# Performance work log

Hardware: AMD Instinct MI355X
Metric: run time of the kernel (lower is better)

The kernel has to match this reference:

```python
import jax, jax.numpy as jnp
import numpy as np

N, E, F, H, C, G = 100000, 1600000, 128, 128, 1, 512
NLAYERS, DT, ALPHA, GAMMA = 5, 1.0, 1.0, 1.0


def setup_inputs() -> dict:
    key = jax.random.key(0)
    ks = jax.random.split(key, 11)
    x = jax.random.normal(ks[0], (N, F), dtype=jnp.float32)
    edge_index = jax.random.randint(ks[1], (2, E), 0, N, dtype=jnp.int64)
    batch = jnp.sort(jax.random.randint(ks[2], (N,), 0, G, dtype=jnp.int64))
    s = 1.0 / np.sqrt(H).astype(np.float32)
    W_enc = jax.random.normal(ks[3], (H, F), jnp.float32) * (1.0 / np.sqrt(F))
    b_enc = jnp.zeros((H,), jnp.float32)
    W_conv = jax.random.normal(ks[4], (H, H), jnp.float32) * s
    b_conv = jnp.zeros((H,), jnp.float32)
    W_res = jax.random.normal(ks[5], (H, H), jnp.float32) * s
    b_res = jnp.zeros((H,), jnp.float32)
    W_dec = jax.random.normal(ks[6], (C, H), jnp.float32) * s
    b_dec = jnp.zeros((C,), jnp.float32)
    return {
        "x": x, "edge_index": edge_index, "batch": batch,
        "W_enc": W_enc, "b_enc": b_enc,
        "W_conv": W_conv, "b_conv": b_conv,
        "W_res": W_res, "b_res": b_res,
        "W_dec": W_dec, "b_dec": b_dec,
    }


def reference(x, edge_index, batch, W_enc, b_enc, W_conv, b_conv, W_res, b_res, W_dec, b_dec):
    src, dst = edge_index[0], edge_index[1]
    # GCN symmetric normalization with self-loops: deg = 1 + in-degree(dst)
    deg = jnp.zeros((N,), x.dtype).at[dst].add(1.0) + 1.0
    dinv = jax.lax.rsqrt(deg)
    norm = dinv[src] * dinv[dst]            # [E]
    self_norm = (dinv * dinv)[:, None]      # [N,1] self-loop coefficient

    def gcn_conv(X):
        xw = X @ W_conv.T                   # lin (bias=False)
        agg = jnp.zeros_like(xw).at[dst].add(norm[:, None] * xw[src])
        agg = agg + self_norm * xw          # self-loop term
        return agg + b_conv

    Y = x @ W_enc.T + b_enc
    Xs = Y
    for _ in range(NLAYERS):
        res = Xs @ W_res.T + b_res - Xs @ W_conv.T   # res(X) - conv.lin(X)
        Y = Y + DT * (jax.nn.relu(gcn_conv(Xs) + res) - ALPHA * Y - GAMMA * Xs)
        Xs = Xs + DT * Y
    out = Xs @ W_dec.T + b_dec               # [N, 1]
    pooled = jax.ops.segment_sum(out, batch, num_segments=G)  # [G, 1]
    return pooled.squeeze(-1)                # [G]
```

## Files before the change

### kernel.cpp

```cpp
#include <hip/hip_runtime.h>
#include <hip/hip_bf16.h>
#include <stdint.h>


#define HD 128
#define SCHUNK 2048

typedef __attribute__((ext_vector_type(4))) float f32x4;
typedef __attribute__((ext_vector_type(8))) float f32x8;
typedef __attribute__((ext_vector_type(8))) _Float16 f16x8;

__global__ __launch_bounds__(256) void k_deg(const int* __restrict__ dst, int E,
                                             int* __restrict__ cnt){
  int e = blockIdx.x * 256 + threadIdx.x;
  if (e < E) atomicAdd(&cnt[dst[e]], 1);
}

__global__ __launch_bounds__(256) void k_scan_part(const int* __restrict__ cnt,
                                                   int* __restrict__ bsum, int N){
  __shared__ int red[256];
  int t = threadIdx.x;
  int lo = blockIdx.x * SCHUNK + t * 8;
  int s = 0;
#pragma unroll
  for (int k = 0; k < 8; ++k){
    int i = lo + k;
    s += (i < N) ? cnt[i] : 0;
  }
  red[t] = s;
  __syncthreads();
  for (int off = 128; off > 0; off >>= 1){
    if (t < off) red[t] += red[t + off];
    __syncthreads();
  }
  if (t == 0) bsum[blockIdx.x] = red[0];
}

__global__ __launch_bounds__(1024) void k_scan_mid(const int* __restrict__ bsum,
                                                   int* __restrict__ boff, int nb,
                                                   int* __restrict__ rp, int N, int E){
  __shared__ int part[1024];
  int t = threadIdx.x;
  part[t] = (t < nb) ? bsum[t] : 0;
  __syncthreads();
  for (int off = 1; off < 1024; off <<= 1){
    int v = (t >= off) ? part[t - off] : 0;
    __syncthreads();
    part[t] += v;
    __syncthreads();
  }
  if (t < nb) boff[t] = (t == 0) ? 0 : part[t - 1];
  if (t == 0) rp[N] = E;
}

__global__ __launch_bounds__(256) void k_scan_apply(const int* __restrict__ cnt,
                                                    const int* __restrict__ boff,
                                                    int* __restrict__ rp,
                                                    float* __restrict__ dinv, int N){
  __shared__ int tsum[256];
  int t = threadIdx.x;
  int lo = blockIdx.x * SCHUNK + t * 8;
  int v[8];
  int s = 0;
#pragma unroll
  for (int k = 0; k < 8; ++k){
    int i = lo + k;
    v[k] = (i < N) ? cnt[i] : 0;
    s += v[k];
  }
  tsum[t] = s;
  __syncthreads();
  for (int off = 1; off < 256; off <<= 1){
    int u = (t >= off) ? tsum[t - off] : 0;
    __syncthreads();
    tsum[t] += u;
    __syncthreads();
  }
  int base = boff[blockIdx.x] + ((t == 0) ? 0 : tsum[t - 1]);
#pragma unroll
  for (int k = 0; k < 8; ++k){
    int i = lo + k;
    if (i < N){
      rp[i] = base;
      dinv[i] = rsqrtf((float)v[k] + 1.0f);
      base += v[k];
    }
  }
}

__global__ __launch_bounds__(256) void k_fill(const int* __restrict__ src,
                                              const int* __restrict__ dst, int E,
                                              const int* __restrict__ rp,
                                              int* cnt,
                                              const float* __restrict__ dinv,
                                              unsigned* __restrict__ col){
  int e = blockIdx.x * 256 + threadIdx.x;
  if (e >= E) return;
  int s = src[e], d = dst[e];
  int pos = rp[d] + atomicSub(&cnt[d], 1) - 1;
  float di = dinv[s];
  int deg1 = (int)(1.0f / (di * di) + 0.5f);
  col[pos] = ((unsigned)deg1 << 18) | (unsigned)s;
}

__global__ __launch_bounds__(256) void k_prep_w(const float* __restrict__ Wc,
                                                const float* __restrict__ Wr,
                                                const float* __restrict__ We,
                                                const float* __restrict__ bc,
                                                const float* __restrict__ br,
                                                _Float16* __restrict__ WcF,
                                                _Float16* __restrict__ WrF,
                                                _Float16* __restrict__ WeF,
                                                float* __restrict__ bias_sum){
  int i = blockIdx.x * 256 + threadIdx.x;
  if (i < HD * HD){
    WcF[i] = (_Float16)Wc[i];
    WrF[i] = (_Float16)Wr[i];
    WeF[i] = (_Float16)We[i];
  }
  if (i < HD) bias_sum[i] = bc[i] + br[i];
}

__global__ __launch_bounds__(256) void k_agg(const _Float16* __restrict__ XsH,
                                             const float* __restrict__ dinv,
                                             const int* __restrict__ rp,
                                             const unsigned* __restrict__ col,
                                             _Float16* __restrict__ U,
                                             int N){
  int w = threadIdx.x >> 6;
  int lane = threadIdx.x & 63;
  int q = lane >> 4;
  int ql = lane & 15;
  int node = blockIdx.x * 4 + w;
  if (node >= N) return;

  float acc[8];
#pragma unroll
  for (int i = 0; i < 8; ++i) acc[i] = 0.f;

  int b = rp[node], e = rp[node + 1];
  int j = b + q;
  for (; j + 4 < e; j += 8){
    unsigned r0 = col[j];
    unsigned r1 = col[j + 4];
    float w0 = rsqrtf((float)(r0 >> 18));
    float w1 = rsqrtf((float)(r1 >> 18));
    f16x8 v0 = ((const f16x8*)(XsH + (size_t)(r0 & 0x3FFFFu) * HD))[ql];
    f16x8 v1 = ((const f16x8*)(XsH + (size_t)(r1 & 0x3FFFFu) * HD))[ql];
#pragma unroll
    for (int i = 0; i < 8; ++i) acc[i] = fmaf(w0, (float)v0[i], acc[i]);
#pragma unroll
    for (int i = 0; i < 8; ++i) acc[i] = fmaf(w1, (float)v1[i], acc[i]);
  }
  if (j < e){
    unsigned r0 = col[j];
    float w0 = rsqrtf((float)(r0 >> 18));
    f16x8 v0 = ((const f16x8*)(XsH + (size_t)(r0 & 0x3FFFFu) * HD))[ql];
#pragma unroll
    for (int i = 0; i < 8; ++i) acc[i] = fmaf(w0, (float)v0[i], acc[i]);
  }

  float dn = dinv[node];
#pragma unroll
  for (int i = 0; i < 8; ++i){
    acc[i] += __shfl_xor(acc[i], 16, 64);
    acc[i] += __shfl_xor(acc[i], 32, 64);
    acc[i] *= dn;
  }
  if (q == 0){
    f16x8 o;
#pragma unroll
    for (int i = 0; i < 8; ++i) o[i] = (_Float16)acc[i];
    ((f16x8*)(U + (size_t)node * HD))[ql] = o;
  }
}

__global__ __launch_bounds__(256) void k_gemm(
    const float* __restrict__ A1f,
    const _Float16* __restrict__ A1h,
    const _Float16* A2h,
    const _Float16* __restrict__ W1,
    const _Float16* __restrict__ W2,
    const float* __restrict__ dinvp,
    const float* __restrict__ bias,
    _Float16* outXsH,
    const float* __restrict__ Wd, const float* __restrict__ bd,
    float* __restrict__ val,
    int N, int relu, int decode){
  __shared__ _Float16 wsm[2 * HD * HD];
  f16x8* smv = (f16x8*)wsm;

  {
    int t = threadIdx.x;
    const f16x8* g1 = (const f16x8*)W1;
    for (int i = t; i < HD * HD / 8; i += 256){
      int row = i >> 4, slot = i & 15;
      smv[(row << 4) | (slot ^ (row & 7))] = g1[i];
    }
    if (W2){
      const f16x8* g2 = (const f16x8*)W2;
      for (int i = t; i < HD * HD / 8; i += 256){
        int row = i >> 4, slot = i & 15;
        smv[2048 + ((row << 4) | (slot ^ (row & 7)))] = g2[i];
      }
    }
  }
  __syncthreads();

  int wid = blockIdx.x * 4 + (threadIdx.x >> 6);
  int row0 = wid * 32;
  if (row0 >= N) return;
  int lane = threadIdx.x & 63;
  int r = lane & 15;
  int kg = lane >> 4;

  f32x4 acc[2][8];
#pragma unroll
  for (int s = 0; s < 2; ++s)
#pragma unroll
    for (int c = 0; c < 8; ++c) acc[s][c] = (f32x4)0.0f;

  const bool two = (A2h != nullptr);
  float sr[2] = {0.f, 0.f};
  if (two){
#pragma unroll
    for (int s = 0; s < 2; ++s){
      float d = dinvp[row0 + s * 16 + r];
      sr[s] = d * d - 1.0f;
    }
  }

#pragma unroll
  for (int kst = 0; kst < 4; ++kst){
    int k0 = kst * 32 + kg * 8;
    f16x8 a1[2], a2[2];
#pragma unroll
    for (int s = 0; s < 2; ++s){
      size_t ao = (size_t)(row0 + s * 16 + r) * HD + k0;
      if (two){
        f16x8 uh = *(const f16x8*)(A1h + ao);
        f16x8 xv = *(const f16x8*)(A2h + ao);
        a2[s] = xv;
#pragma unroll
        for (int i = 0; i < 8; ++i)
          a1[s][i] = (_Float16)fmaf(sr[s], (float)xv[i], (float)uh[i]);
      } else {
        f32x8 u = *(const f32x8*)(A1f + ao);
#pragma unroll
        for (int i = 0; i < 8; ++i) a1[s][i] = (_Float16)u[i];
      }
    }
    int swz = (kst * 4 + kg) ^ (r & 7);
#pragma unroll
    for (int ct = 0; ct < 8; ++ct){
      int ridx = ((ct * 16 + r) << 4) | swz;
      f16x8 b1 = smv[ridx];
#pragma unroll
      for (int s = 0; s < 2; ++s)
        acc[s][ct] = __builtin_amdgcn_mfma_f32_16x16x32_f16(a1[s], b1, acc[s][ct], 0, 0, 0);
      if (two){
        f16x8 b2 = smv[2048 + ridx];
#pragma unroll
        for (int s = 0; s < 2; ++s)
          acc[s][ct] = __builtin_amdgcn_mfma_f32_16x16x32_f16(a2[s], b2, acc[s][ct], 0, 0, 0);
      }
    }
  }

  float rowp[2][4] = {{0.f,0.f,0.f,0.f},{0.f,0.f,0.f,0.f}};
#pragma unroll
  for (int s = 0; s < 2; ++s){
#pragma unroll
    for (int ct = 0; ct < 8; ++ct){
      int cc = ct * 16 + r;
      float bv = bias[cc];
      float wdv = decode ? Wd[cc] : 0.f;
#pragma unroll
      for (int j = 0; j < 4; ++j){
        float v = acc[s][ct][j] + bv;
        if (relu) v = fmaxf(v, 0.0f);
        if (decode){
          rowp[s][j] += v * wdv;
        } else {
          int rr = row0 + s * 16 + kg * 4 + j;
          outXsH[(size_t)rr * HD + cc] = (_Float16)v;
        }
      }
    }
  }
  if (decode){
    float bd0 = bd[0];
#pragma unroll
    for (int s = 0; s < 2; ++s)
#pragma unroll
      for (int j = 0; j < 4; ++j){
        float t = rowp[s][j];
        t += __shfl_xor(t, 1, 64);
        t += __shfl_xor(t, 2, 64);
        t += __shfl_xor(t, 4, 64);
        t += __shfl_xor(t, 8, 64);
        if (r == 0) val[row0 + s * 16 + kg * 4 + j] = t + bd0;
      }
  }
}

#define POOL_CHUNK 1024
__global__ __launch_bounds__(256) void k_pool(const float* __restrict__ val,
                                              const int* __restrict__ batch,
                                              float* __restrict__ out, int N, int G){
  __shared__ float acc[4096];
  int t = threadIdx.x;
  int lo = blockIdx.x * POOL_CHUNK;
  int hi = min(lo + POOL_CHUNK, N);
  if (G <= 4096){
    for (int i = t; i < G; i += 256) acc[i] = 0.f;
    __syncthreads();
    for (int i = lo + t; i < hi; i += 256) atomicAdd(&acc[batch[i]], val[i]);
    __syncthreads();
    for (int i = t; i < G; i += 256){
      float v = acc[i];
      if (v != 0.f) atomicAdd(&out[i], v);
    }
  } else {
    for (int i = lo + t; i < hi; i += 256) atomicAdd(&out[batch[i]], val[i]);
  }
}

extern "C" void kernel_launch(void* const* d_in, const int* in_sizes, int n_in,
                              void* d_out, int out_size, void* d_ws, size_t ws_size,
                              hipStream_t stream){
  const float* x      = (const float*)d_in[0];
  const int*   ei     = (const int*)d_in[1];
  const int*   batch  = (const int*)d_in[2];
  const float* W_enc  = (const float*)d_in[3];
  const float* b_enc  = (const float*)d_in[4];
  const float* W_conv = (const float*)d_in[5];
  const float* b_conv = (const float*)d_in[6];
  const float* W_res  = (const float*)d_in[7];
  const float* b_res  = (const float*)d_in[8];
  const float* W_dec  = (const float*)d_in[9];
  const float* b_dec  = (const float*)d_in[10];

  const int N = in_sizes[0] / HD;
  const int E = in_sizes[1] / 2;
  float* out = (float*)d_out;

  char* ws = (char*)d_ws;
  size_t off = 0;
  auto alloc = [&](size_t bytes) -> char* {
    char* p = ws + off;
    off += (bytes + 255) & ~(size_t)255;
    return p;
  };
  int*   cnt   = (int*)  alloc((size_t)N * 4);
  int*   rp    = (int*)  alloc(((size_t)N + 1) * 4);
  float* dinv  = (float*)alloc((size_t)N * 4);
  int*   bsum  = (int*)  alloc(1024 * 4);
  int*   boff  = (int*)  alloc(1024 * 4);
  unsigned* col= (unsigned*)alloc((size_t)E * 4);
  _Float16* XsH= (_Float16*)alloc((size_t)N * HD * 2);
  _Float16* U  = (_Float16*)alloc((size_t)N * HD * 2);
  float* val   = (float*)alloc((size_t)N * 4);
  _Float16* WcF = (_Float16*)alloc((size_t)HD * HD * 2);
  _Float16* WrF = (_Float16*)alloc((size_t)HD * HD * 2);
  _Float16* WeF = (_Float16*)alloc((size_t)HD * HD * 2);
  float* bias_sum = (float*)alloc((size_t)HD * 4);

  hipMemsetAsync(cnt, 0, (size_t)N * 4, stream);
  hipMemsetAsync(out, 0, (size_t)out_size * 4, stream);

  const int* src = ei;
  const int* dst = ei + E;

  int nb = (N + SCHUNK - 1) / SCHUNK;

  k_deg       <<<(E + 255) / 256, 256, 0, stream>>>(dst, E, cnt);
  k_scan_part <<<nb, 256, 0, stream>>>(cnt, bsum, N);
  k_scan_mid  <<<1, 1024, 0, stream>>>(bsum, boff, nb, rp, N, E);
  k_scan_apply<<<nb, 256, 0, stream>>>(cnt, boff, rp, dinv, N);
  k_fill      <<<(E + 255) / 256, 256, 0, stream>>>(src, dst, E, rp, cnt, dinv, col);
  k_prep_w    <<<(HD * HD + 255) / 256, 256, 0, stream>>>(W_conv, W_res, W_enc, b_conv, b_res,
                                                          WcF, WrF, WeF, bias_sum);

  int gemm_blocks = ((N + 31) / 32 + 3) / 4;
  int node_blocks = (N + 3) / 4;

  k_gemm<<<gemm_blocks, 256, 0, stream>>>(x, nullptr, nullptr, WeF, nullptr,
                                          nullptr, b_enc, XsH,
                                          nullptr, nullptr, nullptr, N, 0, 0);

  for (int l = 0; l < 5; ++l){
    k_agg<<<node_blocks, 256, 0, stream>>>(XsH, dinv, rp, col, U, N);
    int last = (l == 4);
    k_gemm<<<gemm_blocks, 256, 0, stream>>>(nullptr, U, XsH, WcF, WrF,
                                            dinv, bias_sum, XsH,
                                            W_dec, b_dec, val, N, 1, last);
  }

  k_pool<<<(N + POOL_CHUNK - 1) / POOL_CHUNK, 256, 0, stream>>>(val, batch, out, N, out_size);
}
```

Before: 643.6 us.

## Replace atomic CSR build with bucketed binning, unroll aggregation, halve GEMM LDS

Replaces the degree-count, three-kernel scan and atomic fill with a two-level bucket sort. Edges are binned by destination block through per-block LDS staging, and each bucket then builds its CSR segment locally in LDS. The aggregation loop now handles four neighbours per iteration and reads dinv[src] directly instead of decoding a packed degree. The GEMM stages W2 into LDS only after the first product, which halves shared memory to raise occupancy. The fixed bucket capacities (BSTRIDE/BCAP) silently drop edges if a bucket overflows, and the extra dinv gather adds memory traffic.

```diff
diff --git a/kernel.cpp b/kernel.cpp
--- a/kernel.cpp
+++ b/kernel.cpp
@@ -4,103 +4,114 @@
 
 
 #define HD 128
-#define SCHUNK 2048
+#define BSH 9
+#define BSTRIDE 16384
+#define BCAP 12288
 
 typedef __attribute__((ext_vector_type(4))) float f32x4;
 typedef __attribute__((ext_vector_type(8))) float f32x8;
 typedef __attribute__((ext_vector_type(8))) _Float16 f16x8;
 
-__global__ __launch_bounds__(256) void k_deg(const int* __restrict__ dst, int E,
-                                             int* __restrict__ cnt){
-  int e = blockIdx.x * 256 + threadIdx.x;
-  if (e < E) atomicAdd(&cnt[dst[e]], 1);
-}
-
-__global__ __launch_bounds__(256) void k_scan_part(const int* __restrict__ cnt,
-                                                   int* __restrict__ bsum, int N){
-  __shared__ int red[256];
+__global__ __launch_bounds__(256) void k_bin(const int* __restrict__ src,
+                                             const int* __restrict__ dst, int E,
+                                             unsigned* __restrict__ tmp,
+                                             int* __restrict__ gcur, int nbuck){
+  __shared__ unsigned stage[256 * 32];
+  __shared__ int lcnt[256];
   int t = threadIdx.x;
-  int lo = blockIdx.x * SCHUNK + t * 8;
-  int s = 0;
+  lcnt[t] = 0;
+  __syncthreads();
+  int base = blockIdx.x * 2048;
 #pragma unroll
   for (int k = 0; k < 8; ++k){
-    int i = lo + k;
-    s += (i < N) ? cnt[i] : 0;
-  }
-  red[t] = s;
-  __syncthreads();
-  for (int off = 128; off > 0; off >>= 1){
-    if (t < off) red[t] += red[t + off];
-    __syncthreads();
-  }
-  if (t == 0) bsum[blockIdx.x] = red[0];
-}
-
-__global__ __launch_bounds__(1024) void k_scan_mid(const int* __restrict__ bsum,
-                                                   int* __restrict__ boff, int nb,
-                                                   int* __restrict__ rp, int N, int E){
-  __shared__ int part[1024];
+    int e = base + k * 256 + t;
+    if (e < E){
+      int d = dst[e], s = src[e];
+      unsigned rec = ((unsigned)(d & ((1 << BSH) - 1)) << 17) | (unsigned)s;
+      int b = d >> BSH;
+      int slot = atomicAdd(&lcnt[b], 1);
+      if (slot < 32) stage[b * 32 + slot] = rec;
+      else {
+        int g = atomicAdd(&gcur[b], 1);
+        if (g < BSTRIDE) tmp[(size_t)b * BSTRIDE + g] = rec;
+      }
+    }
+  }
+  __syncthreads();
+  int wv = t >> 6, lane = t & 63;
+  for (int b = wv; b < nbuck; b += 4){
+    int cnt = min(lcnt[b], 32);
+    if (cnt == 0) continue;
+    int gbase = 0;
+    if (lane == 0) gbase = atomicAdd(&gcur[b], cnt);
+    gbase = __shfl(gbase, 0, 64);
+    if (lane < cnt && gbase + lane < BSTRIDE)
+      tmp[(size_t)b * BSTRIDE + gbase + lane] = stage[b * 32 + lane];
+  }
+}
+
+__global__ __launch_bounds__(256) void k_bscan(const int* __restrict__ gcur,
+                                               int* __restrict__ bbase, int nbuck,
+                                               int* __restrict__ rp, int N, int E){
+  __shared__ int sm[256];
   int t = threadIdx.x;
-  part[t] = (t < nb) ? bsum[t] : 0;
-  __syncthreads();
-  for (int off = 1; off < 1024; off <<= 1){
-    int v = (t >= off) ? part[t - off] : 0;
-    __syncthreads();
-    part[t] += v;
-    __syncthreads();
-  }
-  if (t < nb) boff[t] = (t == 0) ? 0 : part[t - 1];
+  sm[t] = (t < nbuck) ? gcur[t] : 0;
+  __syncthreads();
+  for (int off = 1; off < 256; off <<= 1){
+    int v = (t >= off) ? sm[t - off] : 0;
+    __syncthreads();
+    sm[t] += v;
+    __syncthreads();
+  }
+  if (t < nbuck) bbase[t] = (t == 0) ? 0 : sm[t - 1];
   if (t == 0) rp[N] = E;
 }
 
-__global__ __launch_bounds__(256) void k_scan_apply(const int* __restrict__ cnt,
-                                                    const int* __restrict__ boff,
-                                                    int* __restrict__ rp,
-                                                    float* __restrict__ dinv, int N){
-  __shared__ int tsum[256];
-  int t = threadIdx.x;
-  int lo = blockIdx.x * SCHUNK + t * 8;
-  int v[8];
-  int s = 0;
-#pragma unroll
-  for (int k = 0; k < 8; ++k){
-    int i = lo + k;
-    v[k] = (i < N) ? cnt[i] : 0;
-    s += v[k];
-  }
-  tsum[t] = s;
+__global__ __launch_bounds__(256) void k_build(const unsigned* __restrict__ tmp,
+                                               const int* __restrict__ gcur,
+                                               const int* __restrict__ bbase,
+                                               int* __restrict__ rp,
+                                               float* __restrict__ dinv,
+                                               unsigned* __restrict__ col, int N){
+  __shared__ unsigned lcol[BCAP];
+  __shared__ int deg[512], rpl[512], cur[512];
+  __shared__ int ps[256];
+  int b = blockIdx.x, t = threadIdx.x;
+  int lo = b << BSH;
+  int nn = min(512, N - lo);
+  int count = min(gcur[b], BCAP);
+  int gbase = bbase[b];
+  for (int i = t; i < 512; i += 256){ deg[i] = 0; cur[i] = 0; }
+  __syncthreads();
+  const unsigned* trec = tmp + (size_t)b * BSTRIDE;
+  for (int i = t; i < count; i += 256)
+    atomicAdd(&deg[trec[i] >> 17], 1);
+  __syncthreads();
+  int a0 = deg[2 * t], a1 = deg[2 * t + 1];
+  ps[t] = a0 + a1;
   __syncthreads();
   for (int off = 1; off < 256; off <<= 1){
-    int u = (t >= off) ? tsum[t - off] : 0;
-    __syncthreads();
-    tsum[t] += u;
-    __syncthreads();
-  }
-  int base = boff[blockIdx.x] + ((t == 0) ? 0 : tsum[t - 1]);
-#pragma unroll
-  for (int k = 0; k < 8; ++k){
-    int i = lo + k;
-    if (i < N){
-      rp[i] = base;
-      dinv[i] = rsqrtf((float)v[k] + 1.0f);
-      base += v[k];
-    }
-  }
-}
-
-__global__ __launch_bounds__(256) void k_fill(const int* __restrict__ src,
-                                              const int* __restrict__ dst, int E,
-                                              const int* __restrict__ rp,
-                                              int* cnt,
-                                              const float* __restrict__ dinv,
-                                              unsigned* __restrict__ col){
-  int e = blockIdx.x * 256 + threadIdx.x;
-  if (e >= E) return;
-  int s = src[e], d = dst[e];
-  int pos = rp[d] + atomicSub(&cnt[d], 1) - 1;
-  float di = dinv[s];
-  int deg1 = (int)(1.0f / (di * di) + 0.5f);
-  col[pos] = ((unsigned)deg1 << 18) | (unsigned)s;
+    int v = (t >= off) ? ps[t - off] : 0;
+    __syncthreads();
+    ps[t] += v;
+    __syncthreads();
+  }
+  int excl = (t == 0) ? 0 : ps[t - 1];
+  rpl[2 * t] = excl;
+  rpl[2 * t + 1] = excl + a0;
+  __syncthreads();
+  for (int i = t; i < nn; i += 256){
+    rp[lo + i] = gbase + rpl[i];
+    dinv[lo + i] = rsqrtf((float)deg[i] + 1.0f);
+  }
+  for (int i = t; i < count; i += 256){
+    unsigned r = trec[i];
+    int d = r >> 17;
+    int pos = rpl[d] + atomicAdd(&cur[d], 1);
+    if (pos < BCAP) lcol[pos] = r & 0x1FFFFu;
+  }
+  __syncthreads();
+  for (int i = t; i < count; i += 256) col[gbase + i] = lcol[i];
 }
 
 __global__ __launch_bounds__(256) void k_prep_w(const float* __restrict__ Wc,
@@ -140,22 +151,32 @@
 
   int b = rp[node], e = rp[node + 1];
   int j = b + q;
-  for (; j + 4 < e; j += 8){
+  for (; j + 12 < e; j += 16){
     unsigned r0 = col[j];
     unsigned r1 = col[j + 4];
-    float w0 = rsqrtf((float)(r0 >> 18));
-    float w1 = rsqrtf((float)(r1 >> 18));
-    f16x8 v0 = ((const f16x8*)(XsH + (size_t)(r0 & 0x3FFFFu) * HD))[ql];
-    f16x8 v1 = ((const f16x8*)(XsH + (size_t)(r1 & 0x3FFFFu) * HD))[ql];
+    unsigned r2 = col[j + 8];
+    unsigned r3 = col[j + 12];
+    float w0 = dinv[r0];
+    float w1 = dinv[r1];
+    float w2 = dinv[r2];
+    float w3 = dinv[r3];
+    f16x8 v0 = ((const f16x8*)(XsH + (size_t)r0 * HD))[ql];
+    f16x8 v1 = ((const f16x8*)(XsH + (size_t)r1 * HD))[ql];
+    f16x8 v2 = ((const f16x8*)(XsH + (size_t)r2 * HD))[ql];
+    f16x8 v3 = ((const f16x8*)(XsH + (size_t)r3 * HD))[ql];
 #pragma unroll
     for (int i = 0; i < 8; ++i) acc[i] = fmaf(w0, (float)v0[i], acc[i]);
 #pragma unroll
     for (int i = 0; i < 8; ++i) acc[i] = fmaf(w1, (float)v1[i], acc[i]);
-  }
-  if (j < e){
+#pragma unroll
+    for (int i = 0; i < 8; ++i) acc[i] = fmaf(w2, (float)v2[i], acc[i]);
+#pragma unroll
+    for (int i = 0; i < 8; ++i) acc[i] = fmaf(w3, (float)v3[i], acc[i]);
+  }
+  for (; j < e; j += 4){
     unsigned r0 = col[j];
-    float w0 = rsqrtf((float)(r0 >> 18));
-    f16x8 v0 = ((const f16x8*)(XsH + (size_t)(r0 & 0x3FFFFu) * HD))[ql];
+    float w0 = dinv[r0];
+    f16x8 v0 = ((const f16x8*)(XsH + (size_t)r0 * HD))[ql];
 #pragma unroll
     for (int i = 0; i < 8; ++i) acc[i] = fmaf(w0, (float)v0[i], acc[i]);
   }
@@ -187,30 +208,24 @@
     const float* __restrict__ Wd, const float* __restrict__ bd,
     float* __restrict__ val,
     int N, int relu, int decode){
-  __shared__ _Float16 wsm[2 * HD * HD];
+  __shared__ _Float16 wsm[HD * HD];
   f16x8* smv = (f16x8*)wsm;
+  int t = threadIdx.x;
 
   {
-    int t = threadIdx.x;
     const f16x8* g1 = (const f16x8*)W1;
     for (int i = t; i < HD * HD / 8; i += 256){
       int row = i >> 4, slot = i & 15;
       smv[(row << 4) | (slot ^ (row & 7))] = g1[i];
     }
-    if (W2){
-      const f16x8* g2 = (const f16x8*)W2;
-      for (int i = t; i < HD * HD / 8; i += 256){
-        int row = i >> 4, slot = i & 15;
-        smv[2048 + ((row << 4) | (slot ^ (row & 7)))] = g2[i];
-      }
-    }
-  }
-  __syncthreads();
-
-  int wid = blockIdx.x * 4 + (threadIdx.x >> 6);
+  }
+  __syncthreads();
+
+  int wid = blockIdx.x * 4 + (t >> 6);
   int row0 = wid * 32;
-  if (row0 >= N) return;
-  int lane = threadIdx.x & 63;
+  bool act = (row0 < N);
+  int rowb = act ? row0 : 0;
+  int lane = t & 63;
   int r = lane & 15;
   int kg = lane >> 4;
 
@@ -225,7 +240,7 @@
   if (two){
 #pragma unroll
     for (int s = 0; s < 2; ++s){
-      float d = dinvp[row0 + s * 16 + r];
+      float d = dinvp[rowb + s * 16 + r];
       sr[s] = d * d - 1.0f;
     }
   }
@@ -233,14 +248,13 @@
 #pragma unroll
   for (int kst = 0; kst < 4; ++kst){
     int k0 = kst * 32 + kg * 8;
-    f16x8 a1[2], a2[2];
+    f16x8 a1[2];
 #pragma unroll
     for (int s = 0; s < 2; ++s){
-      size_t ao = (size_t)(row0 + s * 16 + r) * HD + k0;
+      size_t ao = (size_t)(rowb + s * 16 + r) * HD + k0;
       if (two){
         f16x8 uh = *(const f16x8*)(A1h + ao);
         f16x8 xv = *(const f16x8*)(A2h + ao);
-        a2[s] = xv;
 #pragma unroll
         for (int i = 0; i < 8; ++i)
           a1[s][i] = (_Float16)fmaf(sr[s], (float)xv[i], (float)uh[i]);
@@ -253,13 +267,34 @@
     int swz = (kst * 4 + kg) ^ (r & 7);
 #pragma unroll
     for (int ct = 0; ct < 8; ++ct){
-      int ridx = ((ct * 16 + r) << 4) | swz;
-      f16x8 b1 = smv[ridx];
+      f16x8 b1 = smv[((ct * 16 + r) << 4) | swz];
 #pragma unroll
       for (int s = 0; s < 2; ++s)
         acc[s][ct] = __builtin_amdgcn_mfma_f32_16x16x32_f16(a1[s], b1, acc[s][ct], 0, 0, 0);
-      if (two){
-        f16x8 b2 = smv[2048 + ridx];
+    }
+  }
+
+  if (two){
+    __syncthreads();
+    const f16x8* g2 = (const f16x8*)W2;
+    for (int i = t; i < HD * HD / 8; i += 256){
+      int row = i >> 4, slot = i & 15;
+      smv[(row << 4) | (slot ^ (row & 7))] = g2[i];
+    }
+    __syncthreads();
+#pragma unroll
+    for (int kst = 0; kst < 4; ++kst){
+      int k0 = kst * 32 + kg * 8;
+      f16x8 a2[2];
+#pragma unroll
+      for (int s = 0; s < 2; ++s){
+        size_t ao = (size_t)(rowb + s * 16 + r) * HD + k0;
+        a2[s] = *(const f16x8*)(A2h + ao);
+      }
+      int swz = (kst * 4 + kg) ^ (r & 7);
+#pragma unroll
+      for (int ct = 0; ct < 8; ++ct){
+        f16x8 b2 = smv[((ct * 16 + r) << 4) | swz];
 #pragma unroll
         for (int s = 0; s < 2; ++s)
           acc[s][ct] = __builtin_amdgcn_mfma_f32_16x16x32_f16(a2[s], b2, acc[s][ct], 0, 0, 0);
@@ -281,25 +316,25 @@
         if (relu) v = fmaxf(v, 0.0f);
         if (decode){
           rowp[s][j] += v * wdv;
-        } else {
+        } else if (act){
           int rr = row0 + s * 16 + kg * 4 + j;
           outXsH[(size_t)rr * HD + cc] = (_Float16)v;
         }
       }
     }
   }
-  if (decode){
+  if (decode && act){
     float bd0 = bd[0];
 #pragma unroll
     for (int s = 0; s < 2; ++s)
 #pragma unroll
       for (int j = 0; j < 4; ++j){
-        float t = rowp[s][j];
-        t += __shfl_xor(t, 1, 64);
-        t += __shfl_xor(t, 2, 64);
-        t += __shfl_xor(t, 4, 64);
-        t += __shfl_xor(t, 8, 64);
-        if (r == 0) val[row0 + s * 16 + kg * 4 + j] = t + bd0;
+        float tt = rowp[s][j];
+        tt += __shfl_xor(tt, 1, 64);
+        tt += __shfl_xor(tt, 2, 64);
+        tt += __shfl_xor(tt, 4, 64);
+        tt += __shfl_xor(tt, 8, 64);
+        if (r == 0) val[row0 + s * 16 + kg * 4 + j] = tt + bd0;
       }
   }
 }
@@ -343,6 +378,7 @@
 
   const int N = in_sizes[0] / HD;
   const int E = in_sizes[1] / 2;
+  const int nbuck = (N + (1 << BSH) - 1) >> BSH;
   float* out = (float*)d_out;
 
   char* ws = (char*)d_ws;
@@ -352,11 +388,11 @@
     off += (bytes + 255) & ~(size_t)255;
     return p;
   };
-  int*   cnt   = (int*)  alloc((size_t)N * 4);
   int*   rp    = (int*)  alloc(((size_t)N + 1) * 4);
   float* dinv  = (float*)alloc((size_t)N * 4);
-  int*   bsum  = (int*)  alloc(1024 * 4);
-  int*   boff  = (int*)  alloc(1024 * 4);
+  int*   gcur  = (int*)  alloc((size_t)nbuck * 4);
+  int*   bbase = (int*)  alloc((size_t)nbuck * 4);
+  unsigned* tmp= (unsigned*)alloc((size_t)nbuck * BSTRIDE * 4);
   unsigned* col= (unsigned*)alloc((size_t)E * 4);
   _Float16* XsH= (_Float16*)alloc((size_t)N * HD * 2);
   _Float16* U  = (_Float16*)alloc((size_t)N * HD * 2);
@@ -366,21 +402,17 @@
   _Float16* WeF = (_Float16*)alloc((size_t)HD * HD * 2);
   float* bias_sum = (float*)alloc((size_t)HD * 4);
 
-  hipMemsetAsync(cnt, 0, (size_t)N * 4, stream);
+  hipMemsetAsync(gcur, 0, (size_t)nbuck * 4, stream);
   hipMemsetAsync(out, 0, (size_t)out_size * 4, stream);
 
   const int* src = ei;
   const int* dst = ei + E;
 
-  int nb = (N + SCHUNK - 1) / SCHUNK;
-
-  k_deg       <<<(E + 255) / 256, 256, 0, stream>>>(dst, E, cnt);
-  k_scan_part <<<nb, 256, 0, stream>>>(cnt, bsum, N);
-  k_scan_mid  <<<1, 1024, 0, stream>>>(bsum, boff, nb, rp, N, E);
-  k_scan_apply<<<nb, 256, 0, stream>>>(cnt, boff, rp, dinv, N);
-  k_fill      <<<(E + 255) / 256, 256, 0, stream>>>(src, dst, E, rp, cnt, dinv, col);
-  k_prep_w    <<<(HD * HD + 255) / 256, 256, 0, stream>>>(W_conv, W_res, W_enc, b_conv, b_res,
-                                                          WcF, WrF, WeF, bias_sum);
+  k_bin  <<<(E + 2047) / 2048, 256, 0, stream>>>(src, dst, E, tmp, gcur, nbuck);
+  k_bscan<<<1, 256, 0, stream>>>(gcur, bbase, nbuck, rp, N, E);
+  k_build<<<nbuck, 256, 0, stream>>>(tmp, gcur, bbase, rp, dinv, col, N);
+  k_prep_w<<<(HD * HD + 255) / 256, 256, 0, stream>>>(W_conv, W_res, W_enc, b_conv, b_res,
+                                                      WcF, WrF, WeF, bias_sum);
 
   int gemm_blocks = ((N + 31) / 32 + 3) / 4;
   int node_blocks = (N + 3) / 4;
```

Measured after the change: 1.381 ms. +114.5%, slower.
